# Optimization experiments

Hardware: AMD Instinct MI355X
Metric: run time of the kernel (lower is better)

## Reference

```python
import jax, jax.numpy as jnp
import numpy as np

N = 3072          # node_num
EPS = 1e-20       # matches sample_gumbel eps
ADJ_P = 0.01      # edge probability for the random DAG


def setup_inputs() -> dict:
    key = jax.random.key(0)
    k1, k2, k3 = jax.random.split(key, 3)
    logits = jax.random.normal(k1, (N,), dtype=jnp.float32)
    # Binary DAG adjacency: strictly upper-triangular Bernoulli(p) so a valid
    # topological order always exists (some unselected node has zero row-sum).
    u = jax.random.uniform(k2, (N, N), dtype=jnp.float32)
    adj_mat = jnp.triu((u < ADJ_P).astype(jnp.float32), k=1)
    uniform_noise = jax.random.uniform(k3, (N,), dtype=jnp.float32)
    return {"logits": logits, "adj_mat": adj_mat, "uniform_noise": uniform_noise}


def reference(logits, adj_mat, uniform_noise):
    n = logits.shape[0]
    # sample_gumbel: -log(-log(u + eps) + eps), added to logits
    gumbel_logits = logits + (-jnp.log(-jnp.log(uniform_noise + EPS) + EPS))

    adj_T = adj_mat.T                 # adj_T[idx] == adj_mat[:, idx]
    rowsum0 = adj_mat.sum(axis=1)     # running row sums (out-degree style)
    neg_inf = jnp.array(-jnp.inf, dtype=gumbel_logits.dtype)

    # The torch loop zeroes row/col of the selected node and recomputes
    # adj.sum(dim=1). Equivalent (exact for this math): maintain rowsum,
    # subtract column of the selected node, and pin the selected row to 0.
    def step(carry, _):
        rowsum, unselected = carry
        zerodin = (rowsum == 0) & unselected
        masked = jnp.where(zerodin, gumbel_logits, neg_inf)
        idx = jnp.argmax(masked)
        unselected = unselected.at[idx].set(False)
        rowsum = (rowsum - adj_T[idx]).at[idx].set(0.0)
        return (rowsum, unselected), (idx, zerodin)

    init = (rowsum0, jnp.ones((n,), dtype=bool))
    _, (idxs, masks) = jax.lax.scan(step, init, None, length=n)

    # integrated_mask[max_node_idx] = zerodin_mask at that step
    integrated_mask = jnp.zeros((n, n), dtype=bool).at[idxs].set(masks)

    # rd[i, j] = exp(logits[j] - logits[i]) * mask[i, j]
    rd = jnp.exp(logits[None, :] - logits[:, None]) * integrated_mask
    log_prob = -jnp.log(rd.sum(axis=1) + 1e-10)
    return (log_prob, gumbel_logits)
```

## Files before the change

### kernel.cpp

```cpp
#include <hip/hip_runtime.h>
#include <math.h>

#define NN 3072
#define EPSG 1e-20f
#define EDGE_CAP 53248
#define RCH 128
#define NCH 24
typedef unsigned long long u64;

__global__ __launch_bounds__(256) void rowsum_kernel(const float* __restrict__ adj,
                                                     float* __restrict__ rowsum) {
    int row = blockIdx.x;
    const float* r = adj + (size_t)row * NN;
    float s = 0.f;
    for (int c = threadIdx.x; c < NN; c += 256) s += r[c];
#pragma unroll
    for (int off = 32; off > 0; off >>= 1) s += __shfl_down(s, off);
    __shared__ float ps[4];
    if ((threadIdx.x & 63) == 0) ps[threadIdx.x >> 6] = s;
    __syncthreads();
    if (threadIdx.x == 0) rowsum[row] = (ps[0] + ps[1]) + (ps[2] + ps[3]);
}

__global__ __launch_bounds__(256) void cnt_kernel(const float* __restrict__ adj,
                                                  unsigned* __restrict__ cnt) {
    int c = blockIdx.x * 256 + threadIdx.x;
    const float* col = adj + (size_t)(blockIdx.y * RCH) * NN + c;
    unsigned n = 0;
#pragma unroll 4
    for (int i = 0; i < RCH; ++i)
        n += (col[(size_t)i * NN] != 0.0f) ? 1u : 0u;
    cnt[blockIdx.y * NN + c] = n;
}

__global__ __launch_bounds__(256) void colsum_kernel(const unsigned* __restrict__ cnt,
                                                     unsigned* __restrict__ colcnt) {
    int c = blockIdx.x * 256 + threadIdx.x;
    unsigned n = 0;
    for (int by = 0; by < NCH; ++by) n += cnt[by * NN + c];
    colcnt[c] = n;
}

__global__ __launch_bounds__(64) void scan_kernel(const unsigned* __restrict__ colcnt,
                                                  unsigned* __restrict__ eoff) {
    int lane = threadIdx.x;
    unsigned tot = 0;
    for (int k = 0; k < 48; ++k) tot += colcnt[lane * 48 + k];
    unsigned x = tot;
    for (int off = 1; off < 64; off <<= 1) {
        unsigned y = __shfl_up(x, off);
        if (lane >= off) x += y;
    }
    unsigned run = x - tot;
    for (int k = 0; k < 48; ++k) {
        unsigned c = colcnt[lane * 48 + k];
        eoff[lane * 48 + k] = run;
        run += c;
    }
    if (lane == 63) eoff[NN] = run;
}

__global__ __launch_bounds__(256) void choff_kernel(const unsigned* __restrict__ cnt,
                                                    const unsigned* __restrict__ eoff,
                                                    unsigned* __restrict__ choff) {
    int c = blockIdx.x * 256 + threadIdx.x;
    unsigned run = eoff[c];
    for (int by = 0; by < NCH; ++by) {
        choff[by * NN + c] = run;
        run += cnt[by * NN + c];
    }
}

__global__ __launch_bounds__(256) void fill2_kernel(const float* __restrict__ adj,
                                                    const unsigned* __restrict__ choff,
                                                    unsigned short* __restrict__ edges) {
    int c = blockIdx.x * 256 + threadIdx.x;
    int r0 = blockIdx.y * RCH;
    unsigned off = choff[blockIdx.y * NN + c];
    const float* col = adj + (size_t)r0 * NN + c;
    for (int i = 0; i < RCH; ++i) {
        if (col[(size_t)i * NN] != 0.0f) {
            if (off < EDGE_CAP) edges[off] = (unsigned short)(r0 + i);
            ++off;
        }
    }
}

__device__ __forceinline__ unsigned enc32(float v) {
    unsigned u = __float_as_uint(v);
    return (u & 0x80000000u) ? ~u : (u | 0x80000000u);
}

__global__ __launch_bounds__(256) void gumbel_kernel(const float* __restrict__ logits,
                                                     const float* __restrict__ unif,
                                                     const float* __restrict__ rowsum,
                                                     float* __restrict__ out,
                                                     float* __restrict__ elog,
                                                     unsigned* __restrict__ keyenc,
                                                     unsigned* __restrict__ indeg) {
    int j = blockIdx.x * 256 + threadIdx.x;
    float lg = logits[j];
    float u  = unif[j];
    float g  = lg + (-logf(-logf(u + EPSG) + EPSG));
    out[NN + j] = g;
    elog[j] = expf(lg);
    keyenc[j] = enc32(g);
    indeg[j] = (unsigned)(int)rowsum[j];
}

__global__ __launch_bounds__(256) void rank_kernel(const unsigned* __restrict__ keyenc,
                                                   unsigned* __restrict__ rank,
                                                   unsigned* __restrict__ perm) {
    int j = blockIdx.x;
    unsigned kj = keyenc[j];
    unsigned cnt = 0;
    for (int i = threadIdx.x; i < NN; i += 256) {
        unsigned ki = keyenc[i];
        cnt += (ki > kj || (ki == kj && i < j)) ? 1u : 0u;
    }
#pragma unroll
    for (int off = 32; off > 0; off >>= 1) cnt += __shfl_down(cnt, off);
    __shared__ unsigned ps[4];
    if ((threadIdx.x & 63) == 0) ps[threadIdx.x >> 6] = cnt;
    __syncthreads();
    if (threadIdx.x == 0) {
        unsigned r = ps[0] + ps[1] + ps[2] + ps[3];
        rank[j] = r;
        perm[r] = (unsigned)j;
    }
}

__global__ __launch_bounds__(256) void scatter_kernel(const unsigned* __restrict__ rank,
                                                      const unsigned* __restrict__ eoff,
                                                      const float* __restrict__ elog,
                                                      const unsigned* __restrict__ indeg,
                                                      unsigned* __restrict__ metaR,
                                                      float* __restrict__ elogR,
                                                      unsigned* __restrict__ indegR) {
    int j = blockIdx.x * 256 + threadIdx.x;
    unsigned r = rank[j];
    unsigned e0 = eoff[j];
    unsigned d = eoff[j + 1] - e0;
    metaR[r] = e0 | (d << 20);
    elogR[r] = elog[j];
    indegR[r] = indeg[j];
}

__global__ __launch_bounds__(256) void etrans_kernel(const unsigned short* __restrict__ edges,
                                                     const unsigned* __restrict__ rank,
                                                     unsigned short* __restrict__ edgesR) {
    int i = blockIdx.x * 256 + threadIdx.x;
    if (i < EDGE_CAP + 128) {
        unsigned e = edges[i];
        e = e < NN ? e : NN - 1;
        edgesR[i] = (unsigned short)rank[e];
    }
}

__device__ __forceinline__ float wsum_f32(float v) {
    int t;
    t = __builtin_amdgcn_update_dpp(0, __float_as_int(v), 0x111, 0xf, 0xf, true); v += __int_as_float(t);
    t = __builtin_amdgcn_update_dpp(0, __float_as_int(v), 0x112, 0xf, 0xf, true); v += __int_as_float(t);
    t = __builtin_amdgcn_update_dpp(0, __float_as_int(v), 0x114, 0xf, 0xf, true); v += __int_as_float(t);
    t = __builtin_amdgcn_update_dpp(0, __float_as_int(v), 0x118, 0xf, 0xf, true); v += __int_as_float(t);
    t = __builtin_amdgcn_update_dpp(0, __float_as_int(v), 0x142, 0xf, 0xf, true); v += __int_as_float(t);
    t = __builtin_amdgcn_update_dpp(0, __float_as_int(v), 0x143, 0xf, 0xf, true); v += __int_as_float(t);
    return v;
}
__device__ __forceinline__ int rdlane(int v, int l) { return __builtin_amdgcn_readlane(v, l); }
__device__ __forceinline__ u64 rdlane64(u64 v, int l) {
    unsigned lo = (unsigned)rdlane((int)(unsigned)v, l);
    unsigned hi = (unsigned)rdlane((int)(unsigned)(v >> 32), l);
    return ((u64)hi << 32) | lo;
}
__device__ __forceinline__ int div48(int j) { return ((j >> 4) * 21846) >> 16; }

__global__ __launch_bounds__(256) void topo_kernel(const float* __restrict__ elogR,
                                                   const unsigned* __restrict__ indegR,
                                                   const unsigned* __restrict__ metaR,
                                                   const unsigned short* __restrict__ edgesR,
                                                   const unsigned* __restrict__ perm,
                                                   float* __restrict__ gslog,
                                                   unsigned* __restrict__ gssel,
                                                   float* __restrict__ out) {
    __shared__ unsigned       s_indeg[NN];
    __shared__ float          s_elog[NN];
    __shared__ unsigned       s_meta[NN];
    __shared__ unsigned short s_edges[EDGE_CAP + 128];

    const int tid = threadIdx.x;

    for (int x = tid; x < NN / 4; x += 256) {
        ((uint4*)s_indeg)[x] = ((const uint4*)indegR)[x];
        ((float4*)s_elog)[x] = ((const float4*)elogR)[x];
        ((uint4*)s_meta)[x]  = ((const uint4*)metaR)[x];
    }
    for (int x = tid; x < (EDGE_CAP + 128) / 8; x += 256)
        ((uint4*)s_edges)[x] = ((const uint4*)edgesR)[x];
    __syncthreads();
    if (tid >= 64) return;
    const int lane = tid;
    const int base48 = lane * 48;

    u64 mask = 0ULL;
    float S;
    {
        float ssl = 0.f;
        for (int i = 0; i < 48; ++i) {
            int r = base48 + i;
            if (s_indeg[r] == 0u) { mask |= 1ULL << i; ssl += s_elog[r]; }
        }
        float tot = wsum_f32(ssl);
        S = __int_as_float(rdlane(__float_as_int(tot), 63));
    }

    int r_cur;
    {
        u64 ball = __ballot(mask != 0ULL);
        int gl = (int)__ffsll(ball) - 1;
        u64 mg = rdlane64(mask, gl);
        r_cur = gl * 48 + (int)__ffsll(mg) - 1;
    }
    {
        int og = div48(r_cur);
        if (lane == og) mask &= ~(1ULL << (r_cur - 48 * og));
    }
    unsigned m0 = s_meta[r_cur];
    unsigned e0_cur = m0 & 0xFFFFFu;
    int d = (int)(m0 >> 20);
    int ew = (int)s_edges[e0_cur + (lane < d ? lane : 0)];
    float elog_cur = s_elog[r_cur];

    int spec_rank; unsigned e0s; int ds; int ews; float elog_s;
    {
        u64 ball = __ballot(mask != 0ULL);
        u64 bb = ball ? ball : 1ULL;
        int gl = (int)__ffsll(bb) - 1;
        u64 mg = rdlane64(mask, gl);
        u64 mg2 = mg ? mg : 1ULL;
        spec_rank = ball ? (gl * 48 + (int)__ffsll(mg2) - 1) : 0x7FFFFFFF;
        int sc = spec_rank < NN ? spec_rank : 0;
        unsigned ms = s_meta[sc];
        e0s = ms & 0xFFFFFu; ds = (int)(ms >> 20);
        ews = (int)s_edges[e0s + (lane < ds ? lane : 0)];
        elog_s = s_elog[sc];
    }

    for (int t = 0; t < NN; ++t) {
        if (lane == 0) { gslog[t] = S; gssel[t] = (unsigned)r_cur; }

        bool act = lane < d;
        unsigned old = 0xFFFFFFFFu;
        if (act) old = atomicSub(&s_indeg[ew], 1u);
        int pend = (act && old == 1u) ? ew : -1;

        S -= elog_cur;

        int min_ins = 0x7FFFFFFF;
        u64 ib = __ballot(pend >= 0);
        while (ib) {
            int src = (int)__ffsll(ib) - 1; ib &= ib - 1;
            int rr = rdlane(pend, src);
            int og = div48(rr);
            if (lane == og) mask |= 1ULL << (rr - 48 * og);
            min_ins = rr < min_ins ? rr : min_ins;
            S += s_elog[rr];
        }

        if (d > 64) {
            for (int base = 64; base < d; base += 64) {
                int idx = base + lane;
                int p2 = -1;
                if (idx < d) {
                    int rr2 = (int)s_edges[e0_cur + idx];
                    unsigned o2 = atomicSub(&s_indeg[rr2], 1u);
                    if (o2 == 1u) p2 = rr2;
                }
                u64 ib2 = __ballot(p2 >= 0);
                while (ib2) {
                    int src = (int)__ffsll(ib2) - 1; ib2 &= ib2 - 1;
                    int rr = rdlane(p2, src);
                    int og = div48(rr);
                    if (lane == og) mask |= 1ULL << (rr - 48 * og);
                    min_ins = rr < min_ins ? rr : min_ins;
                    S += s_elog[rr];
                }
            }
        }

        int next = spec_rank < min_ins ? spec_rank : min_ins;

        float elog_next; int dn; int ewn; unsigned e0n;
        if (next != spec_rank) {
            int nc = next < NN ? next : 0;
            unsigned m = s_meta[nc];
            e0n = m & 0xFFFFFu; dn = (int)(m >> 20);
            ewn = (int)s_edges[e0n + (lane < dn ? lane : 0)];
            elog_next = s_elog[nc];
        } else { e0n = e0s; dn = ds; ewn = ews; elog_next = elog_s; }

        if (next < NN) {
            int og = div48(next);
            if (lane == og) mask &= ~(1ULL << (next - 48 * og));
        }

        {
            u64 ball = __ballot(mask != 0ULL);
            u64 bb = ball ? ball : 1ULL;
            int gl = (int)__ffsll(bb) - 1;
            u64 mg = rdlane64(mask, gl);
            u64 mg2 = mg ? mg : 1ULL;
            spec_rank = ball ? (gl * 48 + (int)__ffsll(mg2) - 1) : 0x7FFFFFFF;
            int sc = spec_rank < NN ? spec_rank : 0;
            unsigned ms = s_meta[sc];
            e0s = ms & 0xFFFFFu; ds = (int)(ms >> 20);
            ews = (int)s_edges[e0s + (lane < ds ? lane : 0)];
            elog_s = s_elog[sc];
        }

        r_cur = next; d = dn; ew = ewn; e0_cur = e0n; elog_cur = elog_next;
    }

    for (int i = lane; i < NN; i += 64) {
        unsigned rr = gssel[i];
        float Si = gslog[i];
        int node = (int)perm[rr];
        out[node] = -logf((1.0f / s_elog[rr]) * Si + 1e-10f);
    }
}

extern "C" void kernel_launch(void* const* d_in, const int* in_sizes, int n_in,
                              void* d_out, int out_size, void* d_ws, size_t ws_size,
                              hipStream_t stream) {
    const float* logits = (const float*)d_in[0];
    const float* adj    = (const float*)d_in[1];
    const float* unif   = (const float*)d_in[2];
    float* out = (float*)d_out;

    char* ws = (char*)d_ws;
    float*          rowsum = (float*)(ws + 0);
    unsigned*       cnt    = (unsigned*)(ws + 16384);
    unsigned*       colcnt = (unsigned*)(ws + 311296);
    unsigned*       eoff   = (unsigned*)(ws + 323584);
    unsigned*       choff  = (unsigned*)(ws + 339968);
    unsigned short* edges  = (unsigned short*)(ws + 634880);
    float*          elog   = (float*)(ws + 741376);
    unsigned*       keyenc = (unsigned*)(ws + 753664);
    unsigned*       indeg  = (unsigned*)(ws + 765952);
    unsigned*       rank   = (unsigned*)(ws + 778240);
    unsigned*       perm   = (unsigned*)(ws + 790528);
    unsigned*       metaR  = (unsigned*)(ws + 802816);
    float*          elogR  = (float*)(ws + 815104);
    unsigned*       indegR = (unsigned*)(ws + 827392);
    unsigned short* edgesR = (unsigned short*)(ws + 839680);
    float*          gslog  = (float*)(ws + 946432);
    unsigned*       gssel  = (unsigned*)(ws + 958720);

    rowsum_kernel<<<NN, 256, 0, stream>>>(adj, rowsum);
    cnt_kernel<<<dim3(NN / 256, NCH), 256, 0, stream>>>(adj, cnt);
    colsum_kernel<<<NN / 256, 256, 0, stream>>>(cnt, colcnt);
    scan_kernel<<<1, 64, 0, stream>>>(colcnt, eoff);
    choff_kernel<<<NN / 256, 256, 0, stream>>>(cnt, eoff, choff);
    fill2_kernel<<<dim3(NN / 256, NCH), 256, 0, stream>>>(adj, choff, edges);
    gumbel_kernel<<<NN / 256, 256, 0, stream>>>(logits, unif, rowsum, out,
                                                elog, keyenc, indeg);
    rank_kernel<<<NN, 256, 0, stream>>>(keyenc, rank, perm);
    scatter_kernel<<<NN / 256, 256, 0, stream>>>(rank, eoff, elog, indeg,
                                                 metaR, elogR, indegR);
    etrans_kernel<<<(EDGE_CAP + 128 + 255) / 256, 256, 0, stream>>>(edges, rank, edgesR);
    topo_kernel<<<1, 256, 0, stream>>>(elogR, indegR, metaR, edgesR, perm,
                                       gslog, gssel, out);
}
```

Baseline: 1.285 ms.

## Batch up to four speculative node selections per step with rollback

Replaces the one-node-per-iteration topological selection loop with a batched version. Up to four of the lowest-rank ready nodes are picked at once, their edge loads and shared-memory atomic decrements are issued together, and then they are committed in order. If a newly freed node would have outranked a later speculative pick, the remaining picks are rolled back with atomicAdd and their mask bits restored. The aim is to overlap LDS latency across several serial steps. The cost is more registers, extra branching, and rollback work when speculation fails.

```diff
diff --git a/kernel.cpp b/kernel.cpp
--- a/kernel.cpp
+++ b/kernel.cpp
@@ -214,111 +214,116 @@
         S = __int_as_float(rdlane(__float_as_int(tot), 63));
     }
 
-    int r_cur;
-    {
-        u64 ball = __ballot(mask != 0ULL);
-        int gl = (int)__ffsll(ball) - 1;
-        u64 mg = rdlane64(mask, gl);
-        r_cur = gl * 48 + (int)__ffsll(mg) - 1;
-    }
-    {
-        int og = div48(r_cur);
-        if (lane == og) mask &= ~(1ULL << (r_cur - 48 * og));
-    }
-    unsigned m0 = s_meta[r_cur];
-    unsigned e0_cur = m0 & 0xFFFFFu;
-    int d = (int)(m0 >> 20);
-    int ew = (int)s_edges[e0_cur + (lane < d ? lane : 0)];
-    float elog_cur = s_elog[r_cur];
-
-    int spec_rank; unsigned e0s; int ds; int ews; float elog_s;
-    {
-        u64 ball = __ballot(mask != 0ULL);
-        u64 bb = ball ? ball : 1ULL;
-        int gl = (int)__ffsll(bb) - 1;
-        u64 mg = rdlane64(mask, gl);
-        u64 mg2 = mg ? mg : 1ULL;
-        spec_rank = ball ? (gl * 48 + (int)__ffsll(mg2) - 1) : 0x7FFFFFFF;
-        int sc = spec_rank < NN ? spec_rank : 0;
-        unsigned ms = s_meta[sc];
-        e0s = ms & 0xFFFFFu; ds = (int)(ms >> 20);
-        ews = (int)s_edges[e0s + (lane < ds ? lane : 0)];
-        elog_s = s_elog[sc];
-    }
-
-    for (int t = 0; t < NN; ++t) {
-        if (lane == 0) { gslog[t] = S; gssel[t] = (unsigned)r_cur; }
-
-        bool act = lane < d;
-        unsigned old = 0xFFFFFFFFu;
-        if (act) old = atomicSub(&s_indeg[ew], 1u);
-        int pend = (act && old == 1u) ? ew : -1;
-
-        S -= elog_cur;
-
-        int min_ins = 0x7FFFFFFF;
-        u64 ib = __ballot(pend >= 0);
-        while (ib) {
-            int src = (int)__ffsll(ib) - 1; ib &= ib - 1;
-            int rr = rdlane(pend, src);
-            int og = div48(rr);
-            if (lane == og) mask |= 1ULL << (rr - 48 * og);
-            min_ins = rr < min_ins ? rr : min_ins;
-            S += s_elog[rr];
-        }
-
-        if (d > 64) {
-            for (int base = 64; base < d; base += 64) {
-                int idx = base + lane;
-                int p2 = -1;
-                if (idx < d) {
-                    int rr2 = (int)s_edges[e0_cur + idx];
-                    unsigned o2 = atomicSub(&s_indeg[rr2], 1u);
-                    if (o2 == 1u) p2 = rr2;
-                }
-                u64 ib2 = __ballot(p2 >= 0);
-                while (ib2) {
-                    int src = (int)__ffsll(ib2) - 1; ib2 &= ib2 - 1;
-                    int rr = rdlane(p2, src);
+    int t = 0;
+    int guard = 0;
+    while (t < NN) {
+        if (++guard > NN + 8) break;
+
+        int rb0 = 0x7FFFFFFF, rb1 = 0x7FFFFFFF, rb2 = 0x7FFFFFFF, rb3 = 0x7FFFFFFF;
+        int formed = 0;
+        unsigned e00 = 0, e01 = 0, e02 = 0, e03 = 0;
+        int d0 = 0, d1 = 0, d2 = 0, d3 = 0;
+#pragma unroll
+        for (int b = 0; b < 4; ++b) {
+            u64 ball = __ballot(mask != 0ULL);
+            if (ball == 0ULL) break;
+            int gl = (int)__ffsll(ball) - 1;
+            u64 mg = rdlane64(mask, gl);
+            int bit = (int)__ffsll(mg) - 1;
+            int r = gl * 48 + bit;
+            if (lane == gl) mask &= ~(1ULL << bit);
+            unsigned m = s_meta[r];
+            unsigned e0 = m & 0xFFFFFu;
+            int dd = (int)(m >> 20);
+            if (b == 0) { rb0 = r; e00 = e0; d0 = dd; }
+            else if (b == 1) { rb1 = r; e01 = e0; d1 = dd; }
+            else if (b == 2) { rb2 = r; e02 = e0; d2 = dd; }
+            else { rb3 = r; e03 = e0; d3 = dd; }
+            formed = b + 1;
+            if (dd > 64) break;
+        }
+        if (formed == 0) break;
+
+        int ew0 = 0, ew1 = 0, ew2 = 0, ew3 = 0;
+        if (formed > 0) ew0 = (int)s_edges[e00 + (lane < d0 ? lane : 0)];
+        if (formed > 1) ew1 = (int)s_edges[e01 + (lane < d1 ? lane : 0)];
+        if (formed > 2) ew2 = (int)s_edges[e02 + (lane < d2 ? lane : 0)];
+        if (formed > 3) ew3 = (int)s_edges[e03 + (lane < d3 ? lane : 0)];
+
+        unsigned o0 = 0xFFFFFFFFu, o1 = 0xFFFFFFFFu, o2 = 0xFFFFFFFFu, o3 = 0xFFFFFFFFu;
+        if (formed > 0 && lane < d0) o0 = atomicSub(&s_indeg[ew0], 1u);
+        if (formed > 1 && lane < d1) o1 = atomicSub(&s_indeg[ew1], 1u);
+        if (formed > 2 && lane < d2) o2 = atomicSub(&s_indeg[ew2], 1u);
+        if (formed > 3 && lane < d3) o3 = atomicSub(&s_indeg[ew3], 1u);
+
+        int done = formed;
+        int minins = 0x7FFFFFFF;
+#pragma unroll
+        for (int b = 0; b < 4; ++b) {
+            if (b < done) {
+                int rb = b == 0 ? rb0 : b == 1 ? rb1 : b == 2 ? rb2 : rb3;
+                int dd = b == 0 ? d0 : b == 1 ? d1 : b == 2 ? d2 : d3;
+                int ew = b == 0 ? ew0 : b == 1 ? ew1 : b == 2 ? ew2 : ew3;
+                unsigned oo = b == 0 ? o0 : b == 1 ? o1 : b == 2 ? o2 : o3;
+                unsigned e0f = b == 0 ? e00 : b == 1 ? e01 : b == 2 ? e02 : e03;
+
+                if (lane == 0) { gslog[t + b] = S; gssel[t + b] = (unsigned)rb; }
+                S -= s_elog[rb];
+
+                int pend = (lane < dd && oo == 1u) ? ew : -1;
+                u64 ib = __ballot(pend >= 0);
+                while (ib) {
+                    int src = (int)__ffsll(ib) - 1; ib &= ib - 1;
+                    int rr = rdlane(pend, src);
                     int og = div48(rr);
                     if (lane == og) mask |= 1ULL << (rr - 48 * og);
-                    min_ins = rr < min_ins ? rr : min_ins;
+                    minins = rr < minins ? rr : minins;
                     S += s_elog[rr];
                 }
+
+                if (dd > 64) {
+                    for (int base = 64; base < dd; base += 64) {
+                        int idx = base + lane;
+                        int p2 = -1;
+                        if (idx < dd) {
+                            int rr2 = (int)s_edges[e0f + idx];
+                            unsigned oo2 = atomicSub(&s_indeg[rr2], 1u);
+                            if (oo2 == 1u) p2 = rr2;
+                        }
+                        u64 ib2 = __ballot(p2 >= 0);
+                        while (ib2) {
+                            int src = (int)__ffsll(ib2) - 1; ib2 &= ib2 - 1;
+                            int rr = rdlane(p2, src);
+                            int og = div48(rr);
+                            if (lane == og) mask |= 1ULL << (rr - 48 * og);
+                            minins = rr < minins ? rr : minins;
+                            S += s_elog[rr];
+                        }
+                    }
+                }
+
+                if (b + 1 < done) {
+                    int rnext = b == 0 ? rb1 : b == 1 ? rb2 : rb3;
+                    if (minins < rnext) done = b + 1;
+                }
             }
         }
 
-        int next = spec_rank < min_ins ? spec_rank : min_ins;
-
-        float elog_next; int dn; int ewn; unsigned e0n;
-        if (next != spec_rank) {
-            int nc = next < NN ? next : 0;
-            unsigned m = s_meta[nc];
-            e0n = m & 0xFFFFFu; dn = (int)(m >> 20);
-            ewn = (int)s_edges[e0n + (lane < dn ? lane : 0)];
-            elog_next = s_elog[nc];
-        } else { e0n = e0s; dn = ds; ewn = ews; elog_next = elog_s; }
-
-        if (next < NN) {
-            int og = div48(next);
-            if (lane == og) mask &= ~(1ULL << (next - 48 * og));
-        }
-
-        {
-            u64 ball = __ballot(mask != 0ULL);
-            u64 bb = ball ? ball : 1ULL;
-            int gl = (int)__ffsll(bb) - 1;
-            u64 mg = rdlane64(mask, gl);
-            u64 mg2 = mg ? mg : 1ULL;
-            spec_rank = ball ? (gl * 48 + (int)__ffsll(mg2) - 1) : 0x7FFFFFFF;
-            int sc = spec_rank < NN ? spec_rank : 0;
-            unsigned ms = s_meta[sc];
-            e0s = ms & 0xFFFFFu; ds = (int)(ms >> 20);
-            ews = (int)s_edges[e0s + (lane < ds ? lane : 0)];
-            elog_s = s_elog[sc];
-        }
-
-        r_cur = next; d = dn; ew = ewn; e0_cur = e0n; elog_cur = elog_next;
+        if (done < formed) {
+#pragma unroll
+            for (int b = 1; b < 4; ++b) {
+                if (b >= done && b < formed) {
+                    int rb = b == 1 ? rb1 : b == 2 ? rb2 : rb3;
+                    int dd = b == 1 ? d1 : b == 2 ? d2 : d3;
+                    int ew = b == 1 ? ew1 : b == 2 ? ew2 : ew3;
+                    if (lane < dd) atomicAdd(&s_indeg[ew], 1u);
+                    int og = div48(rb);
+                    if (lane == og) mask |= 1ULL << (rb - 48 * og);
+                }
+            }
+        }
+
+        t += done;
     }
 
     for (int i = lane; i < NN; i += 64) {
```

Measured after the change: 1.779 ms. 1.38x slower.

## Replace running softmax sum with interval difference array and two-deep speculation

Applied to the files above, without the earlier changes.

The sequential topo loop no longer keeps a running sum of exp-logits per step. It records, in shared memory, the step at which each node became available and the step at which it was selected. Afterwards a difference array with a prefix scan rebuilds each step's denominator, which drops the shared loads, float adds and global stores from the serial critical path. The loop also prefetches column metadata for the two lowest-ranked ready nodes instead of one, so a miss on the first candidate can still avoid a dependent load. The cost is more register state and branches per iteration, plus a small post-pass with atomics and a scan.

```diff
diff --git a/kernel.cpp b/kernel.cpp
--- a/kernel.cpp
+++ b/kernel.cpp
@@ -157,16 +157,6 @@
     }
 }
 
-__device__ __forceinline__ float wsum_f32(float v) {
-    int t;
-    t = __builtin_amdgcn_update_dpp(0, __float_as_int(v), 0x111, 0xf, 0xf, true); v += __int_as_float(t);
-    t = __builtin_amdgcn_update_dpp(0, __float_as_int(v), 0x112, 0xf, 0xf, true); v += __int_as_float(t);
-    t = __builtin_amdgcn_update_dpp(0, __float_as_int(v), 0x114, 0xf, 0xf, true); v += __int_as_float(t);
-    t = __builtin_amdgcn_update_dpp(0, __float_as_int(v), 0x118, 0xf, 0xf, true); v += __int_as_float(t);
-    t = __builtin_amdgcn_update_dpp(0, __float_as_int(v), 0x142, 0xf, 0xf, true); v += __int_as_float(t);
-    t = __builtin_amdgcn_update_dpp(0, __float_as_int(v), 0x143, 0xf, 0xf, true); v += __int_as_float(t);
-    return v;
-}
 __device__ __forceinline__ int rdlane(int v, int l) { return __builtin_amdgcn_readlane(v, l); }
 __device__ __forceinline__ u64 rdlane64(u64 v, int l) {
     unsigned lo = (unsigned)rdlane((int)(unsigned)v, l);
@@ -175,25 +165,54 @@
 }
 __device__ __forceinline__ int div48(int j) { return ((j >> 4) * 21846) >> 16; }
 
+__device__ __forceinline__ void two_lowest(u64 mask, int& r1, int& r2) {
+    r1 = 0x7FFFFFFF; r2 = 0x7FFFFFFF;
+    u64 ball = __ballot(mask != 0ULL);
+    if (ball) {
+        int gl1 = (int)__ffsll(ball) - 1;
+        u64 mg1 = rdlane64(mask, gl1);
+        int b1 = (int)__ffsll(mg1) - 1;
+        r1 = gl1 * 48 + b1;
+        u64 mg1r = mg1 & (mg1 - 1);
+        if (mg1r) {
+            r2 = gl1 * 48 + (int)__ffsll(mg1r) - 1;
+        } else {
+            u64 ball2 = ball & (ball - 1);
+            if (ball2) {
+                int gl2 = (int)__ffsll(ball2) - 1;
+                u64 mg2 = rdlane64(mask, gl2);
+                r2 = gl2 * 48 + (int)__ffsll(mg2) - 1;
+            }
+        }
+    }
+}
+
 __global__ __launch_bounds__(256) void topo_kernel(const float* __restrict__ elogR,
                                                    const unsigned* __restrict__ indegR,
                                                    const unsigned* __restrict__ metaR,
                                                    const unsigned short* __restrict__ edgesR,
                                                    const unsigned* __restrict__ perm,
-                                                   float* __restrict__ gslog,
-                                                   unsigned* __restrict__ gssel,
                                                    float* __restrict__ out) {
     __shared__ unsigned       s_indeg[NN];
     __shared__ float          s_elog[NN];
     __shared__ unsigned       s_meta[NN];
+    __shared__ unsigned short s_instime[NN];
+    __shared__ unsigned short s_seltime[NN];
     __shared__ unsigned short s_edges[EDGE_CAP + 128];
 
     const int tid = threadIdx.x;
 
     for (int x = tid; x < NN / 4; x += 256) {
-        ((uint4*)s_indeg)[x] = ((const uint4*)indegR)[x];
+        uint4 dg = ((const uint4*)indegR)[x];
+        ((uint4*)s_indeg)[x] = dg;
         ((float4*)s_elog)[x] = ((const float4*)elogR)[x];
         ((uint4*)s_meta)[x]  = ((const uint4*)metaR)[x];
+        ushort4 it;
+        it.x = dg.x ? (unsigned short)NN : 0;
+        it.y = dg.y ? (unsigned short)NN : 0;
+        it.z = dg.z ? (unsigned short)NN : 0;
+        it.w = dg.w ? (unsigned short)NN : 0;
+        ((ushort4*)s_instime)[x] = it;
     }
     for (int x = tid; x < (EDGE_CAP + 128) / 8; x += 256)
         ((uint4*)s_edges)[x] = ((const uint4*)edgesR)[x];
@@ -203,58 +222,40 @@
     const int base48 = lane * 48;
 
     u64 mask = 0ULL;
-    float S;
+    for (int i = 0; i < 48; ++i)
+        if (s_indeg[base48 + i] == 0u) mask |= 1ULL << i;
+
+#define LOAD_COL(r, E0, D, EW)                                         \
+    {                                                                  \
+        int rc_ = (unsigned)(r) < NN ? (r) : 0;                        \
+        unsigned m_ = s_meta[rc_];                                     \
+        E0 = m_ & 0xFFFFFu;                                            \
+        D = ((unsigned)(r) < NN) ? (int)(m_ >> 20) : 0;                \
+        EW = (int)s_edges[E0 + (lane < D ? lane : 0)];                 \
+    }
+
+    int r_cur, rA, rB;
     {
-        float ssl = 0.f;
-        for (int i = 0; i < 48; ++i) {
-            int r = base48 + i;
-            if (s_indeg[r] == 0u) { mask |= 1ULL << i; ssl += s_elog[r]; }
-        }
-        float tot = wsum_f32(ssl);
-        S = __int_as_float(rdlane(__float_as_int(tot), 63));
-    }
-
-    int r_cur;
-    {
-        u64 ball = __ballot(mask != 0ULL);
-        int gl = (int)__ffsll(ball) - 1;
-        u64 mg = rdlane64(mask, gl);
-        r_cur = gl * 48 + (int)__ffsll(mg) - 1;
-    }
-    {
+        int r1, r2;
+        two_lowest(mask, r1, r2);
+        r_cur = r1;
         int og = div48(r_cur);
         if (lane == og) mask &= ~(1ULL << (r_cur - 48 * og));
-    }
-    unsigned m0 = s_meta[r_cur];
-    unsigned e0_cur = m0 & 0xFFFFFu;
-    int d = (int)(m0 >> 20);
-    int ew = (int)s_edges[e0_cur + (lane < d ? lane : 0)];
-    float elog_cur = s_elog[r_cur];
-
-    int spec_rank; unsigned e0s; int ds; int ews; float elog_s;
-    {
-        u64 ball = __ballot(mask != 0ULL);
-        u64 bb = ball ? ball : 1ULL;
-        int gl = (int)__ffsll(bb) - 1;
-        u64 mg = rdlane64(mask, gl);
-        u64 mg2 = mg ? mg : 1ULL;
-        spec_rank = ball ? (gl * 48 + (int)__ffsll(mg2) - 1) : 0x7FFFFFFF;
-        int sc = spec_rank < NN ? spec_rank : 0;
-        unsigned ms = s_meta[sc];
-        e0s = ms & 0xFFFFFu; ds = (int)(ms >> 20);
-        ews = (int)s_edges[e0s + (lane < ds ? lane : 0)];
-        elog_s = s_elog[sc];
-    }
+        two_lowest(mask, rA, rB);
+    }
+    unsigned eC0, eA0, eB0; int dC, dA, dB, ewC, ewA, ewB;
+    LOAD_COL(r_cur, eC0, dC, ewC);
+    LOAD_COL(rA, eA0, dA, ewA);
+    LOAD_COL(rB, eB0, dB, ewB);
 
     for (int t = 0; t < NN; ++t) {
-        if (lane == 0) { gslog[t] = S; gssel[t] = (unsigned)r_cur; }
-
-        bool act = lane < d;
+        if (lane == 0) s_seltime[r_cur] = (unsigned short)t;
+
+        bool act = lane < dC;
         unsigned old = 0xFFFFFFFFu;
-        if (act) old = atomicSub(&s_indeg[ew], 1u);
-        int pend = (act && old == 1u) ? ew : -1;
-
-        S -= elog_cur;
+        if (act) old = atomicSub(&s_indeg[ewC], 1u);
+        int pend = (act && old == 1u) ? ewC : -1;
+        if (pend >= 0) s_instime[pend] = (unsigned short)(t + 1);
 
         int min_ins = 0x7FFFFFFF;
         u64 ib = __ballot(pend >= 0);
@@ -264,17 +265,16 @@
             int og = div48(rr);
             if (lane == og) mask |= 1ULL << (rr - 48 * og);
             min_ins = rr < min_ins ? rr : min_ins;
-            S += s_elog[rr];
-        }
-
-        if (d > 64) {
-            for (int base = 64; base < d; base += 64) {
+        }
+
+        if (dC > 64) {
+            for (int base = 64; base < dC; base += 64) {
                 int idx = base + lane;
                 int p2 = -1;
-                if (idx < d) {
-                    int rr2 = (int)s_edges[e0_cur + idx];
+                if (idx < dC) {
+                    int rr2 = (int)s_edges[eC0 + idx];
                     unsigned o2 = atomicSub(&s_indeg[rr2], 1u);
-                    if (o2 == 1u) p2 = rr2;
+                    if (o2 == 1u) { p2 = rr2; s_instime[rr2] = (unsigned short)(t + 1); }
                 }
                 u64 ib2 = __ballot(p2 >= 0);
                 while (ib2) {
@@ -283,50 +283,62 @@
                     int og = div48(rr);
                     if (lane == og) mask |= 1ULL << (rr - 48 * og);
                     min_ins = rr < min_ins ? rr : min_ins;
-                    S += s_elog[rr];
                 }
             }
         }
 
-        int next = spec_rank < min_ins ? spec_rank : min_ins;
-
-        float elog_next; int dn; int ewn; unsigned e0n;
-        if (next != spec_rank) {
-            int nc = next < NN ? next : 0;
-            unsigned m = s_meta[nc];
-            e0n = m & 0xFFFFFu; dn = (int)(m >> 20);
-            ewn = (int)s_edges[e0n + (lane < dn ? lane : 0)];
-            elog_next = s_elog[nc];
-        } else { e0n = e0s; dn = ds; ewn = ews; elog_next = elog_s; }
-
-        if (next < NN) {
+        if (t + 1 >= NN) break;
+
+        int next = rA < min_ins ? rA : min_ins;
+        {
             int og = div48(next);
             if (lane == og) mask &= ~(1ULL << (next - 48 * og));
         }
-
-        {
-            u64 ball = __ballot(mask != 0ULL);
-            u64 bb = ball ? ball : 1ULL;
-            int gl = (int)__ffsll(bb) - 1;
-            u64 mg = rdlane64(mask, gl);
-            u64 mg2 = mg ? mg : 1ULL;
-            spec_rank = ball ? (gl * 48 + (int)__ffsll(mg2) - 1) : 0x7FFFFFFF;
-            int sc = spec_rank < NN ? spec_rank : 0;
-            unsigned ms = s_meta[sc];
-            e0s = ms & 0xFFFFFu; ds = (int)(ms >> 20);
-            ews = (int)s_edges[e0s + (lane < ds ? lane : 0)];
-            elog_s = s_elog[sc];
-        }
-
-        r_cur = next; d = dn; ew = ewn; e0_cur = e0n; elog_cur = elog_next;
-    }
-
+        bool hitA = (next == rA);
+        if (hitA) { eC0 = eA0; dC = dA; ewC = ewA; }
+        else LOAD_COL(next, eC0, dC, ewC);
+
+        int r1, r2;
+        two_lowest(mask, r1, r2);
+        unsigned nA0, nB0; int ndA, ndB, nAe, nBe;
+        if (r1 == rB)            { nA0 = eB0; ndA = dB; nAe = ewB; }
+        else if (r1 == rA && !hitA) { nA0 = eA0; ndA = dA; nAe = ewA; }
+        else LOAD_COL(r1, nA0, ndA, nAe);
+        if (r2 == rB)            { nB0 = eB0; ndB = dB; nBe = ewB; }
+        else if (r2 == rA && !hitA) { nB0 = eA0; ndB = dA; nBe = ewA; }
+        else LOAD_COL(r2, nB0, ndB, nBe);
+        rA = r1; eA0 = nA0; dA = ndA; ewA = nAe;
+        rB = r2; eB0 = nB0; dB = ndB; ewB = nBe;
+        r_cur = next;
+    }
+
+    float* diff = (float*)s_meta;
+    for (int i = lane; i < NN; i += 64) diff[i] = 0.f;
     for (int i = lane; i < NN; i += 64) {
-        unsigned rr = gssel[i];
-        float Si = gslog[i];
-        int node = (int)perm[rr];
-        out[node] = -logf((1.0f / s_elog[rr]) * Si + 1e-10f);
-    }
+        float e = s_elog[i];
+        int it = (int)s_instime[i];
+        int st = (int)s_seltime[i];
+        atomicAdd(&diff[it], e);
+        if (st + 1 < NN) atomicAdd(&diff[st + 1], -e);
+    }
+    float base = 0.f;
+    for (int c = 0; c < NN / 64; ++c) {
+        float v = diff[c * 64 + lane];
+#pragma unroll
+        for (int off = 1; off < 64; off <<= 1) {
+            float y = __shfl_up(v, off);
+            if (lane >= off) v += y;
+        }
+        v += base;
+        diff[c * 64 + lane] = v;
+        base = __shfl(v, 63);
+    }
+    for (int i = lane; i < NN; i += 64) {
+        int tau = (int)s_seltime[i];
+        float Si = diff[tau];
+        out[perm[i]] = -logf(Si / s_elog[i] + 1e-10f);
+    }
+#undef LOAD_COL
 }
 
 extern "C" void kernel_launch(void* const* d_in, const int* in_sizes, int n_in,
@@ -353,8 +365,6 @@
     float*          elogR  = (float*)(ws + 815104);
     unsigned*       indegR = (unsigned*)(ws + 827392);
     unsigned short* edgesR = (unsigned short*)(ws + 839680);
-    float*          gslog  = (float*)(ws + 946432);
-    unsigned*       gssel  = (unsigned*)(ws + 958720);
 
     rowsum_kernel<<<NN, 256, 0, stream>>>(adj, rowsum);
     cnt_kernel<<<dim3(NN / 256, NCH), 256, 0, stream>>>(adj, cnt);
@@ -368,6 +378,5 @@
     scatter_kernel<<<NN / 256, 256, 0, stream>>>(rank, eoff, elog, indeg,
                                                  metaR, elogR, indegR);
     etrans_kernel<<<(EDGE_CAP + 128 + 255) / 256, 256, 0, stream>>>(edges, rank, edgesR);
-    topo_kernel<<<1, 256, 0, stream>>>(elogR, indegR, metaR, edgesR, perm,
-                                       gslog, gssel, out);
-}
+    topo_kernel<<<1, 256, 0, stream>>>(elogR, indegR, metaR, edgesR, perm, out);
+}
```

Measured after the change: 1.587 ms. 23.5% more time.

## Defer running candidate-sum to post-loop difference-array prefix scan

Applied to the files above, without the earlier changes.

Removes the per-step running sum S of candidate exp-logits from the serial topological loop. Instead it records each node's insertion time and selection time in shared memory, then rebuilds S at each step afterwards with a difference array and a wave prefix scan. The per-step minimum of newly inserted nodes now comes from a DPP wave-min reduction instead of being tracked inside the serial insert loop. Global scratch writes per step are also removed. The cost is extra shared-memory writes per insertion and a float summation order that differs from before.

```diff
diff --git a/kernel.cpp b/kernel.cpp
--- a/kernel.cpp
+++ b/kernel.cpp
@@ -157,16 +157,6 @@
     }
 }
 
-__device__ __forceinline__ float wsum_f32(float v) {
-    int t;
-    t = __builtin_amdgcn_update_dpp(0, __float_as_int(v), 0x111, 0xf, 0xf, true); v += __int_as_float(t);
-    t = __builtin_amdgcn_update_dpp(0, __float_as_int(v), 0x112, 0xf, 0xf, true); v += __int_as_float(t);
-    t = __builtin_amdgcn_update_dpp(0, __float_as_int(v), 0x114, 0xf, 0xf, true); v += __int_as_float(t);
-    t = __builtin_amdgcn_update_dpp(0, __float_as_int(v), 0x118, 0xf, 0xf, true); v += __int_as_float(t);
-    t = __builtin_amdgcn_update_dpp(0, __float_as_int(v), 0x142, 0xf, 0xf, true); v += __int_as_float(t);
-    t = __builtin_amdgcn_update_dpp(0, __float_as_int(v), 0x143, 0xf, 0xf, true); v += __int_as_float(t);
-    return v;
-}
 __device__ __forceinline__ int rdlane(int v, int l) { return __builtin_amdgcn_readlane(v, l); }
 __device__ __forceinline__ u64 rdlane64(u64 v, int l) {
     unsigned lo = (unsigned)rdlane((int)(unsigned)v, l);
@@ -175,17 +165,28 @@
 }
 __device__ __forceinline__ int div48(int j) { return ((j >> 4) * 21846) >> 16; }
 
+__device__ __forceinline__ unsigned wmin_u32(unsigned v) {
+    unsigned t;
+    t = (unsigned)__builtin_amdgcn_update_dpp((int)v, (int)v, 0x111, 0xf, 0xf, false); v = t < v ? t : v;
+    t = (unsigned)__builtin_amdgcn_update_dpp((int)v, (int)v, 0x112, 0xf, 0xf, false); v = t < v ? t : v;
+    t = (unsigned)__builtin_amdgcn_update_dpp((int)v, (int)v, 0x114, 0xf, 0xf, false); v = t < v ? t : v;
+    t = (unsigned)__builtin_amdgcn_update_dpp((int)v, (int)v, 0x118, 0xf, 0xf, false); v = t < v ? t : v;
+    t = (unsigned)__builtin_amdgcn_update_dpp((int)v, (int)v, 0x142, 0xf, 0xf, false); v = t < v ? t : v;
+    t = (unsigned)__builtin_amdgcn_update_dpp((int)v, (int)v, 0x143, 0xf, 0xf, false); v = t < v ? t : v;
+    return v;
+}
+
 __global__ __launch_bounds__(256) void topo_kernel(const float* __restrict__ elogR,
                                                    const unsigned* __restrict__ indegR,
                                                    const unsigned* __restrict__ metaR,
                                                    const unsigned short* __restrict__ edgesR,
                                                    const unsigned* __restrict__ perm,
-                                                   float* __restrict__ gslog,
-                                                   unsigned* __restrict__ gssel,
                                                    float* __restrict__ out) {
     __shared__ unsigned       s_indeg[NN];
     __shared__ float          s_elog[NN];
     __shared__ unsigned       s_meta[NN];
+    __shared__ unsigned short s_instime[NN];
+    __shared__ unsigned short s_seltime[NN];
     __shared__ unsigned short s_edges[EDGE_CAP + 128];
 
     const int tid = threadIdx.x;
@@ -194,6 +195,8 @@
         ((uint4*)s_indeg)[x] = ((const uint4*)indegR)[x];
         ((float4*)s_elog)[x] = ((const float4*)elogR)[x];
         ((uint4*)s_meta)[x]  = ((const uint4*)metaR)[x];
+        ushort4 z; z.x = 0; z.y = 0; z.z = 0; z.w = 0;
+        ((ushort4*)s_instime)[x] = z;
     }
     for (int x = tid; x < (EDGE_CAP + 128) / 8; x += 256)
         ((uint4*)s_edges)[x] = ((const uint4*)edgesR)[x];
@@ -203,16 +206,8 @@
     const int base48 = lane * 48;
 
     u64 mask = 0ULL;
-    float S;
-    {
-        float ssl = 0.f;
-        for (int i = 0; i < 48; ++i) {
-            int r = base48 + i;
-            if (s_indeg[r] == 0u) { mask |= 1ULL << i; ssl += s_elog[r]; }
-        }
-        float tot = wsum_f32(ssl);
-        S = __int_as_float(rdlane(__float_as_int(tot), 63));
-    }
+    for (int i = 0; i < 48; ++i)
+        if (s_indeg[base48 + i] == 0u) mask |= 1ULL << i;
 
     int r_cur;
     {
@@ -229,9 +224,8 @@
     unsigned e0_cur = m0 & 0xFFFFFu;
     int d = (int)(m0 >> 20);
     int ew = (int)s_edges[e0_cur + (lane < d ? lane : 0)];
-    float elog_cur = s_elog[r_cur];
-
-    int spec_rank; unsigned e0s; int ds; int ews; float elog_s;
+
+    int spec_rank; unsigned e0s; int ds; int ews;
     {
         u64 ball = __ballot(mask != 0ULL);
         u64 bb = ball ? ball : 1ULL;
@@ -243,28 +237,26 @@
         unsigned ms = s_meta[sc];
         e0s = ms & 0xFFFFFu; ds = (int)(ms >> 20);
         ews = (int)s_edges[e0s + (lane < ds ? lane : 0)];
-        elog_s = s_elog[sc];
     }
 
     for (int t = 0; t < NN; ++t) {
-        if (lane == 0) { gslog[t] = S; gssel[t] = (unsigned)r_cur; }
+        if (lane == 0) s_seltime[r_cur] = (unsigned short)t;
 
         bool act = lane < d;
         unsigned old = 0xFFFFFFFFu;
         if (act) old = atomicSub(&s_indeg[ew], 1u);
-        int pend = (act && old == 1u) ? ew : -1;
-
-        S -= elog_cur;
-
-        int min_ins = 0x7FFFFFFF;
-        u64 ib = __ballot(pend >= 0);
+        bool ins = act && (old == 1u);
+        int pend = ins ? ew : 0x7FFFFFFF;
+        if (ins) s_instime[ew] = (unsigned short)(t + 1);
+
+        int min_ins = (int)(unsigned)rdlane((int)wmin_u32((unsigned)pend), 63);
+
+        u64 ib = __ballot(ins);
         while (ib) {
             int src = (int)__ffsll(ib) - 1; ib &= ib - 1;
             int rr = rdlane(pend, src);
             int og = div48(rr);
             if (lane == og) mask |= 1ULL << (rr - 48 * og);
-            min_ins = rr < min_ins ? rr : min_ins;
-            S += s_elog[rr];
         }
 
         if (d > 64) {
@@ -274,7 +266,7 @@
                 if (idx < d) {
                     int rr2 = (int)s_edges[e0_cur + idx];
                     unsigned o2 = atomicSub(&s_indeg[rr2], 1u);
-                    if (o2 == 1u) p2 = rr2;
+                    if (o2 == 1u) { p2 = rr2; s_instime[rr2] = (unsigned short)(t + 1); }
                 }
                 u64 ib2 = __ballot(p2 >= 0);
                 while (ib2) {
@@ -283,23 +275,21 @@
                     int og = div48(rr);
                     if (lane == og) mask |= 1ULL << (rr - 48 * og);
                     min_ins = rr < min_ins ? rr : min_ins;
-                    S += s_elog[rr];
                 }
             }
         }
 
         int next = spec_rank < min_ins ? spec_rank : min_ins;
 
-        float elog_next; int dn; int ewn; unsigned e0n;
+        int dn; int ewn; unsigned e0n;
         if (next != spec_rank) {
             int nc = next < NN ? next : 0;
             unsigned m = s_meta[nc];
             e0n = m & 0xFFFFFu; dn = (int)(m >> 20);
             ewn = (int)s_edges[e0n + (lane < dn ? lane : 0)];
-            elog_next = s_elog[nc];
-        } else { e0n = e0s; dn = ds; ewn = ews; elog_next = elog_s; }
-
-        if (next < NN) {
+        } else { e0n = e0s; dn = ds; ewn = ews; }
+
+        if ((unsigned)next < NN) {
             int og = div48(next);
             if (lane == og) mask &= ~(1ULL << (next - 48 * og));
         }
@@ -315,17 +305,36 @@
             unsigned ms = s_meta[sc];
             e0s = ms & 0xFFFFFu; ds = (int)(ms >> 20);
             ews = (int)s_edges[e0s + (lane < ds ? lane : 0)];
-            elog_s = s_elog[sc];
-        }
-
-        r_cur = next; d = dn; ew = ewn; e0_cur = e0n; elog_cur = elog_next;
-    }
-
+        }
+
+        r_cur = next; d = dn; ew = ewn; e0_cur = e0n;
+    }
+
+    float* diff = (float*)s_meta;
+    for (int i = lane; i < NN; i += 64) diff[i] = 0.f;
     for (int i = lane; i < NN; i += 64) {
-        unsigned rr = gssel[i];
-        float Si = gslog[i];
-        int node = (int)perm[rr];
-        out[node] = -logf((1.0f / s_elog[rr]) * Si + 1e-10f);
+        float e = s_elog[i];
+        int it = (int)s_instime[i];
+        int st = (int)s_seltime[i];
+        atomicAdd(&diff[it], e);
+        if (st + 1 < NN) atomicAdd(&diff[st + 1], -e);
+    }
+    float base = 0.f;
+    for (int c = 0; c < NN / 64; ++c) {
+        float v = diff[c * 64 + lane];
+#pragma unroll
+        for (int off = 1; off < 64; off <<= 1) {
+            float y = __shfl_up(v, off);
+            if (lane >= off) v += y;
+        }
+        v += base;
+        diff[c * 64 + lane] = v;
+        base = __shfl(v, 63);
+    }
+    for (int i = lane; i < NN; i += 64) {
+        int tau = (int)s_seltime[i];
+        float Si = diff[tau];
+        out[perm[i]] = -logf(Si / s_elog[i] + 1e-10f);
     }
 }
 
@@ -353,8 +362,6 @@
     float*          elogR  = (float*)(ws + 815104);
     unsigned*       indegR = (unsigned*)(ws + 827392);
     unsigned short* edgesR = (unsigned short*)(ws + 839680);
-    float*          gslog  = (float*)(ws + 946432);
-    unsigned*       gssel  = (unsigned*)(ws + 958720);
 
     rowsum_kernel<<<NN, 256, 0, stream>>>(adj, rowsum);
     cnt_kernel<<<dim3(NN / 256, NCH), 256, 0, stream>>>(adj, cnt);
@@ -368,6 +375,5 @@
     scatter_kernel<<<NN / 256, 256, 0, stream>>>(rank, eoff, elog, indeg,
                                                  metaR, elogR, indegR);
     etrans_kernel<<<(EDGE_CAP + 128 + 255) / 256, 256, 0, stream>>>(edges, rank, edgesR);
-    topo_kernel<<<1, 256, 0, stream>>>(elogR, indegR, metaR, edgesR, perm,
-                                       gslog, gssel, out);
-}
+    topo_kernel<<<1, 256, 0, stream>>>(elogR, indegR, metaR, edgesR, perm, out);
+}
```

Result: slower. 1.372 ms (+6.8%).
